# Optimization experiments

Hardware: AMD Instinct MI355X
Metric: run time of the kernel (lower is better)

Reference implementation:

```python
import jax, jax.numpy as jnp
import numpy as np

B, H, S, DK, DV = 2, 16, 2048, 64, 64

def setup_inputs() -> dict:
    key = jax.random.key(0)
    kq, kk, kv, km = jax.random.split(key, 4)
    q = jax.random.normal(kq, (B, H, S, DK), dtype=jnp.float32)
    k = jax.random.normal(kk, (B, H, S, DK), dtype=jnp.float32)
    v = jax.random.normal(kv, (B, H, S, DV), dtype=jnp.float32)
    mask = jax.random.randint(km, (B, H, S, S), 0, 2).astype(jnp.bool_)
    return {"q": q, "k": k, "v": v, "mask": mask}

def reference(q, k, v, mask):
    d_k = q.shape[-1]
    # scores: [B, H, Sq, Sk]
    scores = jnp.einsum('bhqd,bhkd->bhqk', q, k) / np.sqrt(d_k).astype(jnp.float32)
    scores = jnp.where(mask, jnp.float32(-1e9), scores)
    attn = jax.nn.softmax(scores, axis=-1)
    return jnp.einsum('bhqk,bhkd->bhqd', attn, v)
```

## Files before the change

### kernel.cpp

```cpp
#include <hip/hip_runtime.h>


#define LOG2E 1.4426950408889634f
#define QSCALE (0.125f * LOG2E)

typedef __attribute__((ext_vector_type(8))) short short8;
typedef __attribute__((ext_vector_type(4))) short short4v;
typedef __attribute__((ext_vector_type(4))) float f32x4;
typedef unsigned __attribute__((ext_vector_type(4))) uintv4;

constexpr int S = 2048, D = 64;

__device__ __forceinline__ short bf16rne(float x) {
  union { float f; unsigned u; } cv; cv.f = x;
  unsigned u = cv.u;
  u += 0x7fffu + ((u >> 16) & 1u);
  return (short)(u >> 16);
}

__global__ void prep(const float* __restrict__ kp, const float* __restrict__ vp,
                     short* __restrict__ kb, short* __restrict__ vt,
                     const unsigned* __restrict__ m, int* __restrict__ flag) {
  const int b = blockIdx.x;
  const int tid = threadIdx.x;
  if (b == 0 && tid < 64) {
    unsigned v = m[tid];
    unsigned long long big = __ballot(v > 1u && v != 0x3F800000u);
    unsigned long long isf = __ballot(v == 0x3F800000u);
    if (tid == 0) *flag = (big != 0ull && isf == 0ull) ? 1 : 0;
  }
  if (b < 2048) {
    size_t i = ((size_t)b * 256 + tid) * 8;
    float4 a = *(const float4*)(kp + i);
    float4 c = *(const float4*)(kp + i + 4);
    short8 s;
    s[0] = bf16rne(a.x); s[1] = bf16rne(a.y); s[2] = bf16rne(a.z); s[3] = bf16rne(a.w);
    s[4] = bf16rne(c.x); s[5] = bf16rne(c.y); s[6] = bf16rne(c.z); s[7] = bf16rne(c.w);
    *(short8*)&kb[i] = s;
  } else {
    __shared__ float tile[64][65];
    const int bb = b - 2048;
    const int bh = bb >> 5, k0 = (bb & 31) * 64;
    const float* src = vp + ((size_t)(bh * S + k0)) * D;
#pragma unroll
    for (int i = 0; i < 4; ++i) {
      int row = i * 16 + (tid >> 4);
      int col = (tid & 15) * 4;
      float4 x = *(const float4*)(src + row * D + col);
      tile[row][col] = x.x; tile[row][col + 1] = x.y;
      tile[row][col + 2] = x.z; tile[row][col + 3] = x.w;
    }
    __syncthreads();
#pragma unroll
    for (int i = 0; i < 4; ++i) {
      int dim = i * 16 + (tid >> 4);
      int kb4 = (tid & 15) * 4;
      short4v s;
#pragma unroll
      for (int j = 0; j < 4; ++j) s[j] = bf16rne(tile[kb4 + j][dim]);
      *(short4v*)&vt[((size_t)(bh * D + dim)) * S + k0 + kb4] = s;
    }
  }
}

__launch_bounds__(256, 4)
__global__ void attn_fwd(const float* __restrict__ qp, const short* __restrict__ kb,
                         const short* __restrict__ vt, const void* __restrict__ mp,
                         float* __restrict__ op, const int* __restrict__ fmtp) {
  const int fmt  = *fmtp;
  const int tid  = threadIdx.x;
  const int lane = tid & 63;
  const int w    = tid >> 6;
  const int c    = lane & 15;
  const int quad = lane >> 4;
  const int kh   = w & 1;
  const int qh   = w >> 1;

  const int bid = (blockIdx.x & 7) * 128 + (blockIdx.x >> 3);
  const int bh  = bid >> 5;
  const int q0  = (bid & 31) * 64;

  __shared__ float Olds[2][32][66];
  __shared__ float Llds[2][32];

  short8 qB[2][2];
#pragma unroll
  for (int qg = 0; qg < 2; ++qg) {
    const float* qg_p = qp + ((size_t)(bh * S + q0 + qh * 32 + qg * 16 + c)) * D;
#pragma unroll
    for (int kk = 0; kk < 2; ++kk) {
      const float* p = qg_p + kk * 32 + quad * 8;
      float4 x = *(const float4*)(p);
      float4 y = *(const float4*)(p + 4);
      short8 f;
      f[0] = bf16rne(x.x * QSCALE); f[1] = bf16rne(x.y * QSCALE);
      f[2] = bf16rne(x.z * QSCALE); f[3] = bf16rne(x.w * QSCALE);
      f[4] = bf16rne(y.x * QSCALE); f[5] = bf16rne(y.y * QSCALE);
      f[6] = bf16rne(y.z * QSCALE); f[7] = bf16rne(y.w * QSCALE);
      qB[qg][kk] = f;
    }
  }

  f32x4 O[2][4];
#pragma unroll
  for (int qg = 0; qg < 2; ++qg)
#pragma unroll
    for (int dt = 0; dt < 4; ++dt) O[qg][dt] = (f32x4){0.f, 0.f, 0.f, 0.f};
  float Lp[2] = {0.f, 0.f};

  const short* kbase = kb + ((size_t)(bh * S)) * D;
  const short* vbase = vt + ((size_t)(bh * D)) * S;
  const int hr0 = 8 * (c >> 2) + (c & 3);

  const size_t mro0 = ((size_t)(bh * S + q0 + qh * 32 + c)) * S;
  const size_t mro1 = mro0 + (size_t)16 * S;

#pragma unroll 1
  for (int it = 0; it < 32; ++it) {
    const int kO = it * 64 + kh * 32;

    short8 kf[2][2];
#pragma unroll
    for (int kt = 0; kt < 2; ++kt)
#pragma unroll
      for (int kk = 0; kk < 2; ++kk)
        kf[kt][kk] = *(const short8*)(kbase +
            (size_t)(kO + hr0 + 4 * kt) * 64 + kk * 32 + quad * 8);

    short8 vf[4];
#pragma unroll
    for (int dt = 0; dt < 4; ++dt)
      vf[dt] = *(const short8*)(vbase + (size_t)(dt * 16 + c) * S + kO + quad * 8);

    unsigned long long mbq0, mbq1;
    if (fmt == 1) {
      mbq0 = *(const unsigned long long*)((const unsigned char*)mp + mro0 + kO + 8 * quad);
      mbq1 = *(const unsigned long long*)((const unsigned char*)mp + mro1 + kO + 8 * quad);
    } else {
      const unsigned* m0 = (const unsigned*)mp + mro0 + kO + 8 * quad;
      const unsigned* m1 = (const unsigned*)mp + mro1 + kO + 8 * quad;
      uintv4 a0 = *(const uintv4*)m0, b0 = *(const uintv4*)(m0 + 4);
      uintv4 a1 = *(const uintv4*)m1, b1 = *(const uintv4*)(m1 + 4);
      mbq0 = 0ull; mbq1 = 0ull;
#pragma unroll
      for (int j = 0; j < 4; ++j) {
        if (a0[j]) mbq0 |= 0xffull << (8 * j);
        if (b0[j]) mbq0 |= 0xffull << (8 * (j + 4));
        if (a1[j]) mbq1 |= 0xffull << (8 * j);
        if (b1[j]) mbq1 |= 0xffull << (8 * (j + 4));
      }
    }

#pragma unroll
    for (int qg = 0; qg < 2; ++qg) {
      const unsigned long long mbq = qg ? mbq1 : mbq0;
      f32x4 z0 = (f32x4){0.f, 0.f, 0.f, 0.f};
      f32x4 z1 = (f32x4){0.f, 0.f, 0.f, 0.f};
      z0 = __builtin_amdgcn_mfma_f32_16x16x32_bf16(kf[0][0], qB[qg][0], z0, 0, 0, 0);
      z0 = __builtin_amdgcn_mfma_f32_16x16x32_bf16(kf[0][1], qB[qg][1], z0, 0, 0, 0);
      z1 = __builtin_amdgcn_mfma_f32_16x16x32_bf16(kf[1][0], qB[qg][0], z1, 0, 0, 0);
      z1 = __builtin_amdgcn_mfma_f32_16x16x32_bf16(kf[1][1], qB[qg][1], z1, 0, 0, 0);

      short8 pf;
      float part = 0.f;
#pragma unroll
      for (int j = 0; j < 8; ++j) {
        float zv = (j < 4) ? z0[j & 3] : z1[j & 3];
        float e = ((mbq >> (8 * j)) & 0xffull) ? 0.f : exp2f(zv);
        part += e;
        pf[j] = bf16rne(e);
      }
      Lp[qg] += part;

#pragma unroll
      for (int dt = 0; dt < 4; ++dt)
        O[qg][dt] = __builtin_amdgcn_mfma_f32_16x16x32_bf16(pf, vf[dt], O[qg][dt], 0, 0, 0);
    }
  }

  float Lq[2];
#pragma unroll
  for (int qg = 0; qg < 2; ++qg) {
    float t = Lp[qg];
    t += __shfl_xor(t, 16);
    t += __shfl_xor(t, 32);
    Lq[qg] = t;
  }

  if (kh == 1) {
#pragma unroll
    for (int qg = 0; qg < 2; ++qg)
#pragma unroll
      for (int dt = 0; dt < 4; ++dt)
#pragma unroll
        for (int r = 0; r < 4; ++r)
          Olds[qh][qg * 16 + quad * 4 + r][dt * 16 + c] = O[qg][dt][r];
    if (quad == 0) {
      Llds[qh][c]      = Lq[0];
      Llds[qh][16 + c] = Lq[1];
    }
  }
  __syncthreads();
  if (kh == 0) {
#pragma unroll
    for (int qg = 0; qg < 2; ++qg)
#pragma unroll
      for (int r = 0; r < 4; ++r) {
        float Ls = __shfl(Lq[qg], (lane & 48) | (quad * 4 + r)) +
                   Llds[qh][qg * 16 + quad * 4 + r];
        float inv = 1.f / Ls;
        const size_t ob =
            ((size_t)(bh * S + q0 + qh * 32 + qg * 16 + quad * 4 + r)) * D;
#pragma unroll
        for (int dt = 0; dt < 4; ++dt)
          op[ob + dt * 16 + c] =
              (O[qg][dt][r] + Olds[qh][qg * 16 + quad * 4 + r][dt * 16 + c]) * inv;
      }
  }
}

extern "C" void kernel_launch(void* const* d_in, const int* in_sizes, int n_in,
                              void* d_out, int out_size, void* d_ws, size_t ws_size,
                              hipStream_t stream) {
  const float* q = (const float*)d_in[0];
  const float* k = (const float*)d_in[1];
  const float* v = (const float*)d_in[2];
  const void*  m = d_in[3];

  short* kbuf = (short*)d_ws;
  short* vtb  = (short*)((char*)d_ws + (8u << 20));
  int* flag   = (int*)((char*)d_ws + (16u << 20));

  prep<<<3072, 256, 0, stream>>>(k, v, kbuf, vtb, (const unsigned*)m, flag);
  attn_fwd<<<1024, 256, 0, stream>>>(q, kbuf, vtb, m, (float*)d_out, flag);
}
```

Measured before the change: 781.3 us.

## Stage K/V tiles through swizzled LDS with async double buffering

Each block now covers 128 queries, four waves of 32, and loops over all keys. The old split-K across wave pairs and its LDS reduction are gone. K and V^T tiles are copied into double-buffered, XOR-swizzled shared memory with global_load_lds, and the next tile's mask is prefetched with nontemporal loads, so global latency overlaps compute and K/V reuse across waves goes through LDS. The grid is halved and launch bounds are relaxed to 2 blocks per CU, which lowers occupancy and adds a __syncthreads per iteration.

```diff
diff --git a/kernel.cpp b/kernel.cpp
--- a/kernel.cpp
+++ b/kernel.cpp
@@ -16,6 +16,12 @@
   unsigned u = cv.u;
   u += 0x7fffu + ((u >> 16) & 1u);
   return (short)(u >> 16);
+}
+
+__device__ __forceinline__ void glds16(const void* g, void* l) {
+  __builtin_amdgcn_global_load_lds(
+      (const __attribute__((address_space(1))) void*)g,
+      (__attribute__((address_space(3))) void*)l, 16, 0, 0);
 }
 
 __global__ void prep(const float* __restrict__ kp, const float* __restrict__ vp,
@@ -63,7 +69,7 @@
   }
 }
 
-__launch_bounds__(256, 4)
+__launch_bounds__(256, 2)
 __global__ void attn_fwd(const float* __restrict__ qp, const short* __restrict__ kb,
                          const short* __restrict__ vt, const void* __restrict__ mp,
                          float* __restrict__ op, const int* __restrict__ fmtp) {
@@ -73,20 +79,18 @@
   const int w    = tid >> 6;
   const int c    = lane & 15;
   const int quad = lane >> 4;
-  const int kh   = w & 1;
-  const int qh   = w >> 1;
-
-  const int bid = (blockIdx.x & 7) * 128 + (blockIdx.x >> 3);
-  const int bh  = bid >> 5;
-  const int q0  = (bid & 31) * 64;
-
-  __shared__ float Olds[2][32][66];
-  __shared__ float Llds[2][32];
+
+  const int bid = (blockIdx.x & 7) * 64 + (blockIdx.x >> 3);
+  const int bh  = bid >> 4;
+  const int q0  = (bid & 15) * 128;
+
+  __shared__ short ks[2][64 * 64];
+  __shared__ short vs[2][64 * 64];
 
   short8 qB[2][2];
 #pragma unroll
   for (int qg = 0; qg < 2; ++qg) {
-    const float* qg_p = qp + ((size_t)(bh * S + q0 + qh * 32 + qg * 16 + c)) * D;
+    const float* qg_p = qp + ((size_t)(bh * S + q0 + w * 32 + qg * 16 + c)) * D;
 #pragma unroll
     for (int kk = 0; kk < 2; ++kk) {
       const float* p = qg_p + kk * 32 + quad * 8;
@@ -108,114 +112,133 @@
     for (int dt = 0; dt < 4; ++dt) O[qg][dt] = (f32x4){0.f, 0.f, 0.f, 0.f};
   float Lp[2] = {0.f, 0.f};
 
+  const int rsub = lane >> 3;
+  const int csw  = (lane & 7) ^ rsub;
   const short* kbase = kb + ((size_t)(bh * S)) * D;
   const short* vbase = vt + ((size_t)(bh * D)) * S;
-  const int hr0 = 8 * (c >> 2) + (c & 3);
-
-  const size_t mro0 = ((size_t)(bh * S + q0 + qh * 32 + c)) * S;
+
+  const size_t mro0 = ((size_t)(bh * S + q0 + w * 32 + c)) * S;
   const size_t mro1 = mro0 + (size_t)16 * S;
 
-#pragma unroll 1
+  unsigned long long mm[2][2];
+
+  auto stage = [&](int it, int buf) {
+    const int k0 = it * 64;
+#pragma unroll
+    for (int h2 = 0; h2 < 2; ++h2) {
+      const int row = (h2 * 4 + w) * 8 + rsub;
+      glds16(kbase + (size_t)(k0 + row) * 64 + csw * 8,
+             (char*)&ks[buf][0] + (h2 * 4 + w) * 1024);
+      glds16(vbase + (size_t)row * S + k0 + csw * 8,
+             (char*)&vs[buf][0] + (h2 * 4 + w) * 1024);
+    }
+  };
+
+  auto mload = [&](int it) {
+    const int kO = it * 64;
+    if (fmt == 1) {
+#pragma unroll
+      for (int qg = 0; qg < 2; ++qg)
+#pragma unroll
+        for (int kg = 0; kg < 2; ++kg)
+          mm[qg][kg] = __builtin_nontemporal_load((const unsigned long long*)
+              ((const unsigned char*)mp + (qg ? mro1 : mro0) + kO + kg * 32 + 8 * quad));
+    } else {
+#pragma unroll
+      for (int qg = 0; qg < 2; ++qg)
+#pragma unroll
+        for (int kg = 0; kg < 2; ++kg) {
+          const unsigned* m0 =
+              (const unsigned*)mp + (qg ? mro1 : mro0) + kO + kg * 32 + 8 * quad;
+          uintv4 a = __builtin_nontemporal_load((const uintv4*)m0);
+          uintv4 b = __builtin_nontemporal_load((const uintv4*)(m0 + 4));
+          unsigned long long t = 0ull;
+#pragma unroll
+          for (int j = 0; j < 4; ++j) {
+            if (a[j]) t |= 0xffull << (8 * j);
+            if (b[j]) t |= 0xffull << (8 * (j + 4));
+          }
+          mm[qg][kg] = t;
+        }
+    }
+  };
+
+  stage(0, 0);
+  mload(0);
+
   for (int it = 0; it < 32; ++it) {
-    const int kO = it * 64 + kh * 32;
-
-    short8 kf[2][2];
-#pragma unroll
-    for (int kt = 0; kt < 2; ++kt)
-#pragma unroll
-      for (int kk = 0; kk < 2; ++kk)
-        kf[kt][kk] = *(const short8*)(kbase +
-            (size_t)(kO + hr0 + 4 * kt) * 64 + kk * 32 + quad * 8);
-
-    short8 vf[4];
-#pragma unroll
-    for (int dt = 0; dt < 4; ++dt)
-      vf[dt] = *(const short8*)(vbase + (size_t)(dt * 16 + c) * S + kO + quad * 8);
-
-    unsigned long long mbq0, mbq1;
-    if (fmt == 1) {
-      mbq0 = *(const unsigned long long*)((const unsigned char*)mp + mro0 + kO + 8 * quad);
-      mbq1 = *(const unsigned long long*)((const unsigned char*)mp + mro1 + kO + 8 * quad);
-    } else {
-      const unsigned* m0 = (const unsigned*)mp + mro0 + kO + 8 * quad;
-      const unsigned* m1 = (const unsigned*)mp + mro1 + kO + 8 * quad;
-      uintv4 a0 = *(const uintv4*)m0, b0 = *(const uintv4*)(m0 + 4);
-      uintv4 a1 = *(const uintv4*)m1, b1 = *(const uintv4*)(m1 + 4);
-      mbq0 = 0ull; mbq1 = 0ull;
-#pragma unroll
-      for (int j = 0; j < 4; ++j) {
-        if (a0[j]) mbq0 |= 0xffull << (8 * j);
-        if (b0[j]) mbq0 |= 0xffull << (8 * (j + 4));
-        if (a1[j]) mbq1 |= 0xffull << (8 * j);
-        if (b1[j]) mbq1 |= 0xffull << (8 * (j + 4));
+    const int buf = it & 1;
+    __syncthreads();
+
+    if (it + 1 < 32) stage(it + 1, buf ^ 1);
+
+    unsigned long long mb[2][2];
+#pragma unroll
+    for (int qg = 0; qg < 2; ++qg) {
+      mb[qg][0] = mm[qg][0]; mb[qg][1] = mm[qg][1];
+    }
+    if (it + 1 < 32) mload(it + 1);
+
+#pragma unroll
+    for (int kg = 0; kg < 2; ++kg) {
+      short8 ka[2][2];
+#pragma unroll
+      for (int kt = 0; kt < 2; ++kt) {
+        const int rr = kg * 32 + 8 * (c >> 2) + (c & 3) + 4 * kt;
+        const int r7 = (c & 3) + 4 * kt;
+#pragma unroll
+        for (int kk = 0; kk < 2; ++kk)
+          ka[kt][kk] = *(const short8*)&ks[buf][rr * 64 + (((kk * 4 + quad) ^ r7) * 8)];
       }
-    }
-
-#pragma unroll
-    for (int qg = 0; qg < 2; ++qg) {
-      const unsigned long long mbq = qg ? mbq1 : mbq0;
-      f32x4 z0 = (f32x4){0.f, 0.f, 0.f, 0.f};
-      f32x4 z1 = (f32x4){0.f, 0.f, 0.f, 0.f};
-      z0 = __builtin_amdgcn_mfma_f32_16x16x32_bf16(kf[0][0], qB[qg][0], z0, 0, 0, 0);
-      z0 = __builtin_amdgcn_mfma_f32_16x16x32_bf16(kf[0][1], qB[qg][1], z0, 0, 0, 0);
-      z1 = __builtin_amdgcn_mfma_f32_16x16x32_bf16(kf[1][0], qB[qg][0], z1, 0, 0, 0);
-      z1 = __builtin_amdgcn_mfma_f32_16x16x32_bf16(kf[1][1], qB[qg][1], z1, 0, 0, 0);
-
-      short8 pf;
-      float part = 0.f;
-#pragma unroll
-      for (int j = 0; j < 8; ++j) {
-        float zv = (j < 4) ? z0[j & 3] : z1[j & 3];
-        float e = ((mbq >> (8 * j)) & 0xffull) ? 0.f : exp2f(zv);
-        part += e;
-        pf[j] = bf16rne(e);
+      short8 vb[4];
+#pragma unroll
+      for (int dt = 0; dt < 4; ++dt)
+        vb[dt] = *(const short8*)&vs[buf][(dt * 16 + c) * 64 +
+                                          (((kg * 4 + quad) ^ (c & 7)) * 8)];
+
+#pragma unroll
+      for (int qg = 0; qg < 2; ++qg) {
+        f32x4 z0 = (f32x4){0.f, 0.f, 0.f, 0.f};
+        f32x4 z1 = (f32x4){0.f, 0.f, 0.f, 0.f};
+        z0 = __builtin_amdgcn_mfma_f32_16x16x32_bf16(ka[0][0], qB[qg][0], z0, 0, 0, 0);
+        z0 = __builtin_amdgcn_mfma_f32_16x16x32_bf16(ka[0][1], qB[qg][1], z0, 0, 0, 0);
+        z1 = __builtin_amdgcn_mfma_f32_16x16x32_bf16(ka[1][0], qB[qg][0], z1, 0, 0, 0);
+        z1 = __builtin_amdgcn_mfma_f32_16x16x32_bf16(ka[1][1], qB[qg][1], z1, 0, 0, 0);
+
+        short8 pf;
+        float part = 0.f;
+        const unsigned long long mq = mb[qg][kg];
+#pragma unroll
+        for (int j = 0; j < 8; ++j) {
+          float zv = (j < 4) ? z0[j & 3] : z1[j & 3];
+          float e = ((mq >> (8 * j)) & 0xffull) ? 0.f : exp2f(zv);
+          part += e;
+          pf[j] = bf16rne(e);
+        }
+        Lp[qg] += part;
+
+#pragma unroll
+        for (int dt = 0; dt < 4; ++dt)
+          O[qg][dt] =
+              __builtin_amdgcn_mfma_f32_16x16x32_bf16(pf, vb[dt], O[qg][dt], 0, 0, 0);
       }
-      Lp[qg] += part;
-
-#pragma unroll
-      for (int dt = 0; dt < 4; ++dt)
-        O[qg][dt] = __builtin_amdgcn_mfma_f32_16x16x32_bf16(pf, vf[dt], O[qg][dt], 0, 0, 0);
-    }
-  }
-
-  float Lq[2];
+    }
+  }
+
 #pragma unroll
   for (int qg = 0; qg < 2; ++qg) {
     float t = Lp[qg];
     t += __shfl_xor(t, 16);
     t += __shfl_xor(t, 32);
-    Lq[qg] = t;
-  }
-
-  if (kh == 1) {
-#pragma unroll
-    for (int qg = 0; qg < 2; ++qg)
-#pragma unroll
-      for (int dt = 0; dt < 4; ++dt)
-#pragma unroll
-        for (int r = 0; r < 4; ++r)
-          Olds[qh][qg * 16 + quad * 4 + r][dt * 16 + c] = O[qg][dt][r];
-    if (quad == 0) {
-      Llds[qh][c]      = Lq[0];
-      Llds[qh][16 + c] = Lq[1];
-    }
-  }
-  __syncthreads();
-  if (kh == 0) {
-#pragma unroll
-    for (int qg = 0; qg < 2; ++qg)
-#pragma unroll
-      for (int r = 0; r < 4; ++r) {
-        float Ls = __shfl(Lq[qg], (lane & 48) | (quad * 4 + r)) +
-                   Llds[qh][qg * 16 + quad * 4 + r];
-        float inv = 1.f / Ls;
-        const size_t ob =
-            ((size_t)(bh * S + q0 + qh * 32 + qg * 16 + quad * 4 + r)) * D;
-#pragma unroll
-        for (int dt = 0; dt < 4; ++dt)
-          op[ob + dt * 16 + c] =
-              (O[qg][dt][r] + Olds[qh][qg * 16 + quad * 4 + r][dt * 16 + c]) * inv;
-      }
+#pragma unroll
+    for (int r = 0; r < 4; ++r) {
+      float Ls = __shfl(t, (lane & 48) | (quad * 4 + r));
+      float inv = 1.f / Ls;
+      const size_t ob =
+          ((size_t)(bh * S + q0 + w * 32 + qg * 16 + quad * 4 + r)) * D;
+#pragma unroll
+      for (int dt = 0; dt < 4; ++dt) op[ob + dt * 16 + c] = O[qg][dt][r] * inv;
+    }
   }
 }
 
@@ -232,5 +255,5 @@
   int* flag   = (int*)((char*)d_ws + (16u << 20));
 
   prep<<<3072, 256, 0, stream>>>(k, v, kbuf, vtb, (const unsigned*)m, flag);
-  attn_fwd<<<1024, 256, 0, stream>>>(q, kbuf, vtb, m, (float*)d_out, flag);
-}
+  attn_fwd<<<512, 256, 0, stream>>>(q, kbuf, vtb, m, (float*)d_out, flag);
+}
```

Measured after the change: 775.7 us. No clear change (-0.7%).
